# Kernel optimization log

Measured on AMD Instinct MI355X. Metric: run time of the kernel, lower is better.

Reference implementation:

```python
import jax, jax.numpy as jnp
import numpy as np

# dims
B, NB, T, NC = 16, 55, 512, 8          # batch, filter bands, time steps, CSP comps
D, L, H, E, K, F, C = 512, 6, 8, 8, 2, 2048, 2  # embed, depth, heads, experts, top_k, d_ff, classes
DH = D // H
IN = NB * NC  # 440
EPS = 1e-5


def _ln(x, s, b):
    m = x.mean(-1, keepdims=True)
    v = ((x - m) ** 2).mean(-1, keepdims=True)
    return (x - m) / jnp.sqrt(v + EPS) * s + b


def setup_inputs() -> dict:
    key = jax.random.key(0)
    ks = iter(jax.random.split(key, 64))
    n = lambda shape, s=0.02: jax.random.normal(next(ks), shape, jnp.float32) * s
    inp = {
        "x": jax.random.normal(next(ks), (B, NB, T, NC), jnp.float32),
        # frontend
        "proj_w": n((IN, D)), "proj_b": jnp.zeros((D,), jnp.float32),
        "pos": n((1, T, D)),
        "ln_pre_s": jnp.ones((D,), jnp.float32), "ln_pre_b": jnp.zeros((D,), jnp.float32),
        # stacked transformer-block params [L, ...]
        "ln1_s": jnp.ones((L, D), jnp.float32), "ln1_b": jnp.zeros((L, D), jnp.float32),
        "wq": n((L, D, D)), "bq": jnp.zeros((L, D), jnp.float32),
        "wk": n((L, D, D)), "bk": jnp.zeros((L, D), jnp.float32),
        "wv": n((L, D, D)), "bv": jnp.zeros((L, D), jnp.float32),
        "wo": n((L, D, D)), "bo": jnp.zeros((L, D), jnp.float32),
        "ln2_s": jnp.ones((L, D), jnp.float32), "ln2_b": jnp.zeros((L, D), jnp.float32),
        "gate_w": n((L, D, E)),
        "e_w1": n((L, E, D, F)), "e_b1": jnp.zeros((L, E, F), jnp.float32),
        "e_w2": n((L, E, F, D)), "e_b2": jnp.zeros((L, E, D), jnp.float32),
        # classifier head
        "ln_f_s": jnp.ones((D,), jnp.float32), "ln_f_b": jnp.zeros((D,), jnp.float32),
        "head_w": n((D, C)), "head_b": jnp.zeros((C,), jnp.float32),
    }
    return inp


def _moe(h, gw, w1, b1, w2, b2):
    # h: [N, D]; top-K softmax-gated mixture of GELU-FFN experts + load-balance aux loss
    N = h.shape[0]
    probs = jax.nn.softmax(h @ gw, axis=-1)                  # [N, E]
    vals, idx = jax.lax.top_k(probs, K)                      # [N, K]
    w = vals / vals.sum(-1, keepdims=True)                   # renormalized top-k weights
    disp = jax.nn.one_hot(idx, E, dtype=h.dtype)             # [N, K, E]
    combine = (disp * w[..., None]).sum(1)                   # [N, E]
    y = jnp.zeros_like(h)
    for e in range(E):  # small fixed expert loop
        y = y + combine[:, e:e + 1] * (jax.nn.gelu(h @ w1[e] + b1[e]) @ w2[e] + b2[e])
    frac = disp.mean((0, 1)) * K                             # fraction of tokens routed to each expert
    aux = E * jnp.sum(frac * probs.mean(0))
    return y, aux


def reference(x, proj_w, proj_b, pos, ln_pre_s, ln_pre_b, ln1_s, ln1_b, wq, bq, wk, bk,
              wv, bv, wo, bo, ln2_s, ln2_b, gate_w, e_w1, e_b1, e_w2, e_b2,
              ln_f_s, ln_f_b, head_w, head_b):
    b, nb, t, nc = x.shape
    h = x.transpose(0, 2, 1, 3).reshape(b, t, nb * nc) @ proj_w + proj_b  # [B,T,D]
    h = _ln(h + pos[:, :t, :], ln_pre_s, ln_pre_b)
    scale = DH ** -0.5
    total_aux = jnp.float32(0.0)
    for l in range(L):
        # pre-LN multi-head self-attention
        a = _ln(h, ln1_s[l], ln1_b[l])
        q = (a @ wq[l] + bq[l]).reshape(b, t, H, DH)
        k = (a @ wk[l] + bk[l]).reshape(b, t, H, DH)
        v = (a @ wv[l] + bv[l]).reshape(b, t, H, DH)
        att = jax.nn.softmax(jnp.einsum('bqhd,bkhd->bhqk', q, k) * scale, axis=-1)
        o = jnp.einsum('bhqk,bkhd->bqhd', att, v).reshape(b, t, D) @ wo[l] + bo[l]
        h = h + o
        # pre-LN MoE FFN
        m = _ln(h, ln2_s[l], ln2_b[l]).reshape(b * t, D)
        y, aux = _moe(m, gate_w[l], e_w1[l], e_b1[l], e_w2[l], e_b2[l])
        h = h + y.reshape(b, t, D)
        total_aux = total_aux + aux
    pooled = h.mean(axis=1)                                   # [B, D]
    logits = _ln(pooled, ln_f_s, ln_f_b) @ head_w + head_b    # [B, C]
    return logits, total_aux
```

## Files before the change

### kernel.cpp

```cpp
#include <hip/hip_runtime.h>
#include <stdint.h>

typedef unsigned short u16;
typedef unsigned int   u32;
typedef short bh8 __attribute__((ext_vector_type(8)));
typedef float f4  __attribute__((ext_vector_type(4)));

#define NTOK    8192
#define PADROWS 17408
#define MAXTILES 136

__device__ __forceinline__ u16 f2bf(float f){
  u32 u = __float_as_uint(f);
  return (u16)((u + 0x7fffu + ((u>>16)&1u)) >> 16);
}
__device__ __forceinline__ float bf2f(u16 h){ return __uint_as_float(((u32)h)<<16); }
__device__ __forceinline__ u32 pk2(float a, float b){ return (u32)f2bf(a) | ((u32)f2bf(b)<<16); }
__device__ __forceinline__ float gelu_f(float x){
  float u = 0.7978845608028654f*(x + 0.044715f*x*x*x);
  float t = 1.f - 2.f/(__expf(2.f*u)+1.f);
  return 0.5f*x*(1.f+t);
}
__device__ __forceinline__ void gload_lds16(const void* g, void* l){
  __builtin_amdgcn_global_load_lds((const __attribute__((address_space(1))) u32*)g,
                                   (__attribute__((address_space(3))) u32*)l, 16, 0, 0);
}

__global__ __launch_bounds__(256) void xpose_k(const float* __restrict__ x, u16* __restrict__ xt){
  int idx = blockIdx.x*256 + threadIdx.x;
  const float* src = x + (size_t)idx*8;
  float4 a = *(const float4*)src;
  float4 b = *(const float4*)(src+4);
  int t  = idx & 511;
  int nb = (idx>>9) % 55;
  int bb = (idx>>9) / 55;
  uint4 u;
  u.x = pk2(a.x,a.y); u.y = pk2(a.z,a.w); u.z = pk2(b.x,b.y); u.w = pk2(b.z,b.w);
  *(uint4*)&xt[((size_t)(bb*512+t))*448 + nb*8] = u;
}

__device__ __forceinline__ void tile_xpose(const float* __restrict__ src, u16* __restrict__ dst,
                                           int Ksrc, int N, int Kdst, float (*tile)[65])
{
  int tid = threadIdx.x;
  int k0 = blockIdx.y*64, n0 = blockIdx.x*64;
  #pragma unroll
  for (int p=0;p<4;++p){
    int r = p*16 + (tid>>4);
    int c4 = (tid&15)*4;
    int k = k0 + r;
    float4 v = (k < Ksrc) ? *(const float4*)&src[(size_t)k*N + n0 + c4] : (float4){0.f,0.f,0.f,0.f};
    tile[r][c4]=v.x; tile[r][c4+1]=v.y; tile[r][c4+2]=v.z; tile[r][c4+3]=v.w;
  }
  __syncthreads();
  #pragma unroll
  for (int p=0;p<2;++p){
    int rn = p*32 + (tid>>3);
    int ck = (tid&7)*8;
    uint4 u;
    u.x = pk2(tile[ck+0][rn], tile[ck+1][rn]);
    u.y = pk2(tile[ck+2][rn], tile[ck+3][rn]);
    u.z = pk2(tile[ck+4][rn], tile[ck+5][rn]);
    u.w = pk2(tile[ck+6][rn], tile[ck+7][rn]);
    *(uint4*)&dst[(size_t)(n0+rn)*Kdst + k0 + ck] = u;
  }
}

__global__ __launch_bounds__(256) void wconv_k(const float* __restrict__ src, u16* __restrict__ dst,
                                               int Ksrc, int N, int Kdst){
  __shared__ float tile[64][65];
  src += (size_t)blockIdx.z*Ksrc*N;
  dst += (size_t)blockIdx.z*N*Kdst;
  tile_xpose(src, dst, Ksrc, N, Kdst, tile);
}

__global__ __launch_bounds__(256) void wconv4_k(const float* __restrict__ wq, const float* __restrict__ wk,
    const float* __restrict__ wv, const float* __restrict__ wo,
    u16* __restrict__ qkvt, u16* __restrict__ wot)
{
  __shared__ float tile[64][65];
  int z = blockIdx.z;
  const float* src = (z==0)? wq : (z==1)? wk : (z==2)? wv : wo;
  u16* dst = (z==3) ? wot : qkvt + (size_t)z*512*512;
  tile_xpose(src, dst, 512, 512, 512, tile);
}

__global__ __launch_bounds__(256) void qkvb_k(const float* __restrict__ bq, const float* __restrict__ bk,
                                              const float* __restrict__ bv, float* __restrict__ qkvb){
  int idx = blockIdx.x*256 + threadIdx.x;
  int l = idx/1536, c = idx - l*1536;
  const float* s = (c<512)? bq : (c<1024)? bk : bv;
  qkvb[idx] = s[l*512 + (c&511)];
}

template<int MODE, bool GATHER>
__global__ __launch_bounds__(256) void gemm2_k(
    const u16* __restrict__ A, int lda,
    const u16* __restrict__ Bt, int ldb, int Ksteps,
    const float* __restrict__ biasBase,
    float* __restrict__ Cf, u16* __restrict__ Cb, int ldc,
    const int* __restrict__ tile_e, const int* __restrict__ toklist,
    const int* __restrict__ slotk, const float* __restrict__ wlist,
    int expN)
{
  __shared__ __align__(16) u16 As[128*32];
  __shared__ __align__(16) u16 Bs[128*32];
  const int tid = threadIdx.x, lane = tid&63, w = tid>>6;
  const int wr = w>>1, wc = w&1;
  const int n0 = blockIdx.x*128, m0 = blockIdx.y*128;
  const u16* Bp = Bt;
  const float* bias = biasBase;
  if constexpr (MODE>=3){
    int e = tile_e[blockIdx.y];
    Bp   += (size_t)e*(size_t)expN*(size_t)ldb;
    bias += (size_t)e*(size_t)expN;
  }
  const u16* asrc0; const u16* asrc1; const u16* bsrc0; const u16* bsrc1;
  {
    int idx0 = tid, row0 = idx0>>2, sp0 = idx0&3, ks0 = sp0 ^ ((row0>>1)&3);
    int idx1 = 256+tid, row1 = idx1>>2, sp1 = idx1&3, ks1 = sp1 ^ ((row1>>1)&3);
    size_t ar0 = GATHER ? (size_t)toklist[m0+row0] : (size_t)(m0+row0);
    size_t ar1 = GATHER ? (size_t)toklist[m0+row1] : (size_t)(m0+row1);
    asrc0 = A + ar0*(size_t)lda + ks0*8;
    asrc1 = A + ar1*(size_t)lda + ks1*8;
    bsrc0 = Bp + (size_t)(n0+row0)*ldb + ks0*8;
    bsrc1 = Bp + (size_t)(n0+row1)*ldb + ks1*8;
  }
  f4 acc[4][4];
  #pragma unroll
  for (int i=0;i<4;++i)
    #pragma unroll
    for (int j=0;j<4;++j) acc[i][j] = (f4){0.f,0.f,0.f,0.f};

  for (int kt=0; kt<Ksteps; ++kt){
    gload_lds16(asrc0, &As[tid*8]);
    gload_lds16(asrc1, &As[(256+tid)*8]);
    gload_lds16(bsrc0, &Bs[tid*8]);
    gload_lds16(bsrc1, &Bs[(256+tid)*8]);
    asrc0 += 32; asrc1 += 32; bsrc0 += 32; bsrc1 += 32;
    __syncthreads();
    bh8 af[4], bf[4];
    const int q = lane>>4;
    #pragma unroll
    for (int mf=0;mf<4;++mf){
      int r = wr*64 + mf*16 + (lane&15);
      af[mf] = *(const bh8*)&As[r*32 + (q ^ ((r>>1)&3))*8];
    }
    #pragma unroll
    for (int nf=0;nf<4;++nf){
      int r = wc*64 + nf*16 + (lane&15);
      bf[nf] = *(const bh8*)&Bs[r*32 + (q ^ ((r>>1)&3))*8];
    }
    #pragma unroll
    for (int mf=0;mf<4;++mf)
      #pragma unroll
      for (int nf=0;nf<4;++nf)
        acc[mf][nf] = __builtin_amdgcn_mfma_f32_16x16x32_bf16(af[mf], bf[nf], acc[mf][nf], 0, 0, 0);
    __syncthreads();
  }
  #pragma unroll
  for (int mf=0;mf<4;++mf){
    #pragma unroll
    for (int nf=0;nf<4;++nf){
      f4 d = acc[mf][nf];
      int ncol = n0 + wc*64 + nf*16 + (lane&15);
      float bv = bias[ncol];
      #pragma unroll
      for (int r=0;r<4;++r){
        int mrow = m0 + wr*64 + mf*16 + (lane>>4)*4 + r;
        float val = d[r] + bv;
        if constexpr (MODE==0){
          Cf[(size_t)mrow*ldc + ncol] = val;
        } else if constexpr (MODE==1){
          int slab = ncol>>6, dh = ncol&63;
          Cb[((size_t)slab*NTOK + (size_t)mrow)*64 + dh] = f2bf(val);
        } else if constexpr (MODE==2){
          Cf[(size_t)mrow*ldc + ncol] += val;
        } else if constexpr (MODE==3){
          Cb[(size_t)mrow*ldc + ncol] = f2bf(gelu_f(val));
        } else {
          int sk = slotk[mrow];
          if (sk >= 0){
            int tok = toklist[mrow];
            atomicAdd(&Cf[(size_t)tok*512 + ncol], wlist[mrow]*val);
          }
        }
      }
    }
  }
}

template<bool ADDPOS, bool OUTF32>
__global__ __launch_bounds__(256) void ln_k(const float* __restrict__ X, const float* __restrict__ pos,
    const float* __restrict__ sc, const float* __restrict__ bi,
    float* __restrict__ outF, u16* __restrict__ outB)
{
  int tid=threadIdx.x, lane=tid&63, w=tid>>6;
  int row = blockIdx.x*4 + w;
  const float* xr = X + (size_t)row*512 + lane*8;
  float x[8];
  float4 v0 = *(const float4*)xr;
  float4 v1 = *(const float4*)(xr+4);
  x[0]=v0.x;x[1]=v0.y;x[2]=v0.z;x[3]=v0.w;x[4]=v1.x;x[5]=v1.y;x[6]=v1.z;x[7]=v1.w;
  if constexpr (ADDPOS){
    const float* pr = pos + (size_t)(row&511)*512 + lane*8;
    float4 p0 = *(const float4*)pr, p1 = *(const float4*)(pr+4);
    x[0]+=p0.x;x[1]+=p0.y;x[2]+=p0.z;x[3]+=p0.w;x[4]+=p1.x;x[5]+=p1.y;x[6]+=p1.z;x[7]+=p1.w;
  }
  float sm=0.f, sq=0.f;
  #pragma unroll
  for (int i=0;i<8;++i){ sm+=x[i]; sq+=x[i]*x[i]; }
  #pragma unroll
  for (int mk=1; mk<64; mk<<=1){ sm += __shfl_xor(sm, mk); sq += __shfl_xor(sq, mk); }
  float mean = sm*(1.f/512.f);
  float var  = sq*(1.f/512.f) - mean*mean;
  float rstd = rsqrtf(var + 1e-5f);
  int d0 = lane*8;
  float4 s0 = *(const float4*)(sc+d0), s1 = *(const float4*)(sc+d0+4);
  float4 b0 = *(const float4*)(bi+d0), b1 = *(const float4*)(bi+d0+4);
  float y[8];
  y[0]=(x[0]-mean)*rstd*s0.x+b0.x; y[1]=(x[1]-mean)*rstd*s0.y+b0.y;
  y[2]=(x[2]-mean)*rstd*s0.z+b0.z; y[3]=(x[3]-mean)*rstd*s0.w+b0.w;
  y[4]=(x[4]-mean)*rstd*s1.x+b1.x; y[5]=(x[5]-mean)*rstd*s1.y+b1.y;
  y[6]=(x[6]-mean)*rstd*s1.z+b1.z; y[7]=(x[7]-mean)*rstd*s1.w+b1.w;
  if constexpr (OUTF32){
    float4 o0 = {y[0],y[1],y[2],y[3]}, o1 = {y[4],y[5],y[6],y[7]};
    *(float4*)(outF + (size_t)row*512 + d0)     = o0;
    *(float4*)(outF + (size_t)row*512 + d0 + 4) = o1;
  } else {
    uint4 u; u.x=pk2(y[0],y[1]); u.y=pk2(y[2],y[3]); u.z=pk2(y[4],y[5]); u.w=pk2(y[6],y[7]);
    *(uint4*)&outB[(size_t)row*512 + d0] = u;
  }
}

__global__ __launch_bounds__(256) void attn_k(const u16* __restrict__ QKV, u16* __restrict__ Og)
{
  __shared__ __align__(16) u16 VT[2][64*72];
  __shared__ __align__(16) u16 PS[4][16*72];
  int tid=threadIdx.x, lane=tid&63, w=tid>>6;
  int qt=blockIdx.x, hh=blockIdx.y, bb=blockIdx.z;
  const u16* Qh = QKV + ((size_t)hh     *NTOK + (size_t)bb*512)*64;
  const u16* Kh = QKV + ((size_t)(8+hh) *NTOK + (size_t)bb*512)*64;
  const u16* Vh = QKV + ((size_t)(16+hh)*NTOK + (size_t)bb*512)*64;
  size_t obase = (size_t)bb*512*512 + (size_t)hh*64;
  int qrow0 = qt*64 + w*16;
  bh8 qf[2];
  #pragma unroll
  for (int kf=0;kf<2;++kf)
    qf[kf] = *(const bh8*)&Qh[ (size_t)(qrow0 + (lane&15))*64 + kf*32 + (lane>>4)*8 ];
  f4 oacc[4];
  #pragma unroll
  for (int i=0;i<4;++i) oacc[i] = (f4){0.f,0.f,0.f,0.f};
  float mrun[4] = {-1e30f,-1e30f,-1e30f,-1e30f};
  float lrun[4] = {0.f,0.f,0.f,0.f};
  const float scale = 0.125f;

  for (int kt=0; kt<8; ++kt){
    const int buf = kt&1;
    #pragma unroll
    for (int r2=0;r2<2;++r2){
      int idx = r2*256 + tid;
      int dhg = idx&7;
      int dh0 = dhg*8, key = idx>>3;
      uint4 raw = *(const uint4*)&Vh[ (size_t)(kt*64+key)*64 + dh0 ];
      int kx = key ^ (dhg<<3);
      u32 rw[4] = {raw.x, raw.y, raw.z, raw.w};
      #pragma unroll
      for (int j=0;j<4;++j){
        VT[buf][(dh0+2*j  )*72 + kx] = (u16)(rw[j]&0xffff);
        VT[buf][(dh0+2*j+1)*72 + kx] = (u16)(rw[j]>>16);
      }
    }
    f4 s[4];
    #pragma unroll
    for (int nf=0;nf<4;++nf){
      size_t krow = (size_t)(kt*64+nf*16+(lane&15))*64 + (lane>>4)*8;
      bh8 k0 = *(const bh8*)&Kh[krow];
      bh8 k1 = *(const bh8*)&Kh[krow+32];
      f4 z = (f4){0.f,0.f,0.f,0.f};
      z = __builtin_amdgcn_mfma_f32_16x16x32_bf16(qf[0], k0, z, 0,0,0);
      z = __builtin_amdgcn_mfma_f32_16x16x32_bf16(qf[1], k1, z, 0,0,0);
      s[nf] = z;
    }
    float pe[4][4];
    #pragma unroll
    for (int r=0;r<4;++r){
      float sv0=s[0][r]*scale, sv1=s[1][r]*scale, sv2=s[2][r]*scale, sv3=s[3][r]*scale;
      float mt = fmaxf(fmaxf(sv0,sv1), fmaxf(sv2,sv3));
      #pragma unroll
      for (int mk=1; mk<16; mk<<=1) mt = fmaxf(mt, __shfl_xor(mt, mk));
      float mn = fmaxf(mrun[r], mt);
      float sf = __expf(mrun[r]-mn);
      float p0=__expf(sv0-mn), p1=__expf(sv1-mn), p2=__expf(sv2-mn), p3=__expf(sv3-mn);
      pe[0][r]=p0; pe[1][r]=p1; pe[2][r]=p2; pe[3][r]=p3;
      float rs = p0+p1+p2+p3;
      #pragma unroll
      for (int mk=1; mk<16; mk<<=1) rs += __shfl_xor(rs, mk);
      lrun[r] = lrun[r]*sf + rs;
      mrun[r] = mn;
      #pragma unroll
      for (int df=0;df<4;++df) oacc[df][r] *= sf;
    }
    #pragma unroll
    for (int nf=0;nf<4;++nf)
      #pragma unroll
      for (int r=0;r<4;++r)
        PS[w][ ((lane>>4)*4+r)*72 + nf*16 + (lane&15) ] = f2bf(pe[nf][r]);
    __syncthreads();
    #pragma unroll
    for (int ks=0;ks<2;++ks){
      bh8 pa = *(const bh8*)&PS[w][ (lane&15)*72 + ks*32 + (lane>>4)*8 ];
      #pragma unroll
      for (int df=0;df<4;++df){
        int dh = df*16 + (lane&15);
        int sgrp = (dh>>3)&7;
        bh8 vb = *(const bh8*)&VT[buf][ dh*72 + ((ks*4 + (lane>>4)) ^ sgrp)*8 ];
        oacc[df] = __builtin_amdgcn_mfma_f32_16x16x32_bf16(pa, vb, oacc[df], 0,0,0);
      }
    }
  }
  #pragma unroll
  for (int df=0;df<4;++df)
    #pragma unroll
    for (int r=0;r<4;++r){
      int qr = qrow0 + (lane>>4)*4 + r;
      float ov = oacc[df][r] / lrun[r];
      Og[ obase + (size_t)qr*512 + df*16 + (lane&15) ] = f2bf(ov);
    }
}

__global__ __launch_bounds__(256) void route_k(const u16* __restrict__ m, const float* __restrict__ gw,
    float* __restrict__ psum, int* __restrict__ cnt, int* __restrict__ t2e, float* __restrict__ t2w)
{
  __shared__ float ps[8]; __shared__ int cs[8];
  int tid=threadIdx.x, lane=tid&63, w=tid>>6;
  if (tid<8){ ps[tid]=0.f; cs[tid]=0; }
  __syncthreads();
  for (int it=0; it<4; ++it){
    int t = blockIdx.x*16 + w*4 + it;
    const u16* row = m + (size_t)t*512 + lane*8;
    uint4 raw = *(const uint4*)row;
    u32 rw[4] = {raw.x,raw.y,raw.z,raw.w};
    float x[8];
    #pragma unroll
    for (int j=0;j<4;++j){ x[2*j]=bf2f((u16)(rw[j]&0xffff)); x[2*j+1]=bf2f((u16)(rw[j]>>16)); }
    float acc[8] = {0,0,0,0,0,0,0,0};
    #pragma unroll
    for (int j=0;j<8;++j){
      const float* g = gw + (size_t)(lane*8+j)*8;
      float4 g0 = *(const float4*)g, g1 = *(const float4*)(g+4);
      acc[0]+=x[j]*g0.x; acc[1]+=x[j]*g0.y; acc[2]+=x[j]*g0.z; acc[3]+=x[j]*g0.w;
      acc[4]+=x[j]*g1.x; acc[5]+=x[j]*g1.y; acc[6]+=x[j]*g1.z; acc[7]+=x[j]*g1.w;
    }
    #pragma unroll
    for (int mk=1; mk<64; mk<<=1)
      #pragma unroll
      for (int e=0;e<8;++e) acc[e] += __shfl_xor(acc[e], mk);
    if (lane==0){
      float mx=acc[0];
      #pragma unroll
      for (int e=1;e<8;++e) mx = fmaxf(mx, acc[e]);
      float pe[8], tot=0.f;
      #pragma unroll
      for (int e=0;e<8;++e){ pe[e]=__expf(acc[e]-mx); tot+=pe[e]; }
      float inv = 1.f/tot;
      #pragma unroll
      for (int e=0;e<8;++e) pe[e]*=inv;
      int e0=0; float v0=pe[0];
      #pragma unroll
      for (int e=1;e<8;++e) if (pe[e]>v0){ v0=pe[e]; e0=e; }
      int e1=-1; float v1=-1.f;
      #pragma unroll
      for (int e=0;e<8;++e) if (e!=e0 && pe[e]>v1){ v1=pe[e]; e1=e; }
      float invw = 1.f/(v0+v1);
      t2e[2*t]=e0; t2w[2*t]=v0*invw; t2e[2*t+1]=e1; t2w[2*t+1]=v1*invw;
      #pragma unroll
      for (int e=0;e<8;++e) atomicAdd(&ps[e], pe[e]);
      atomicAdd(&cs[e0],1); atomicAdd(&cs[e1],1);
    }
  }
  __syncthreads();
  if (tid<8){ atomicAdd(&psum[tid], ps[tid]); atomicAdd(&cnt[tid], cs[tid]); }
}

__global__ __launch_bounds__(256) void offsets_k(const int* __restrict__ cnt, const float* __restrict__ psum,
    int* __restrict__ offs, int* __restrict__ fill, int* __restrict__ tile_e,
    int* __restrict__ toklist, int* __restrict__ slotk, float* __restrict__ wlist, float* __restrict__ auxp)
{
  int tid = threadIdx.x;
  if (tid==0){
    int off=0; float auxl=0.f;
    for (int e=0;e<8;++e){
      offs[e] = off;
      int reg = (cnt[e]+127)&~127;
      int t0 = off>>7, t1 = (off+reg)>>7;
      for (int t=t0;t<t1;++t) tile_e[t]=e;
      off += reg;
      auxl += ((float)cnt[e]*(1.f/8192.f)) * (psum[e]*(1.f/8192.f));
    }
    for (int t=off>>7; t<MAXTILES; ++t) tile_e[t]=0;
    auxp[0] += 8.f*auxl;
  }
  if (tid<8) fill[tid]=0;
  for (int i=tid;i<PADROWS;i+=256){ toklist[i]=0; slotk[i]=-1; wlist[i]=0.f; }
}

__global__ __launch_bounds__(256) void scatter_k(const int* __restrict__ t2e, const float* __restrict__ t2w,
    const int* __restrict__ offs, int* __restrict__ fill,
    int* __restrict__ toklist, int* __restrict__ slotk, float* __restrict__ wlist)
{
  int t = blockIdx.x*256 + threadIdx.x;
  #pragma unroll
  for (int kk=0;kk<2;++kk){
    int e = t2e[2*t+kk];
    int p = atomicAdd(&fill[e], 1);
    int i = offs[e] + p;
    toklist[i] = t; slotk[i] = kk; wlist[i] = t2w[2*t+kk];
  }
}

__global__ __launch_bounds__(256) void pool_k(const float* __restrict__ h, float* __restrict__ pooled){
  int idx = blockIdx.x*256 + threadIdx.x;
  int bb = idx>>9, d = idx&511;
  const float* p = h + (size_t)bb*512*512 + d;
  float s=0.f;
  for (int t=0;t<512;++t) s += p[(size_t)t*512];
  pooled[idx] = s*(1.f/512.f);
}

__global__ __launch_bounds__(256) void head_k(const float* __restrict__ pooled,
    const float* __restrict__ sc, const float* __restrict__ bi,
    const float* __restrict__ hw, const float* __restrict__ hb,
    const float* __restrict__ auxp, float* __restrict__ out)
{
  int tid=threadIdx.x, lane=tid&63, w=tid>>6;
  for (int i=0;i<4;++i){
    int row = w*4+i;
    const float* xr = pooled + (size_t)row*512 + lane*8;
    float x[8];
    float4 v0 = *(const float4*)xr, v1 = *(const float4*)(xr+4);
    x[0]=v0.x;x[1]=v0.y;x[2]=v0.z;x[3]=v0.w;x[4]=v1.x;x[5]=v1.y;x[6]=v1.z;x[7]=v1.w;
    float sm=0.f, sq=0.f;
    #pragma unroll
    for (int j=0;j<8;++j){ sm+=x[j]; sq+=x[j]*x[j]; }
    #pragma unroll
    for (int mk=1; mk<64; mk<<=1){ sm += __shfl_xor(sm, mk); sq += __shfl_xor(sq, mk); }
    float mean = sm*(1.f/512.f);
    float rstd = rsqrtf(sq*(1.f/512.f) - mean*mean + 1e-5f);
    int d0 = lane*8;
    float c0=0.f, c1=0.f;
    #pragma unroll
    for (int j=0;j<8;++j){
      float yv = (x[j]-mean)*rstd*sc[d0+j] + bi[d0+j];
      c0 += yv*hw[(d0+j)*2]; c1 += yv*hw[(d0+j)*2+1];
    }
    #pragma unroll
    for (int mk=1; mk<64; mk<<=1){ c0 += __shfl_xor(c0, mk); c1 += __shfl_xor(c1, mk); }
    if (lane==0){ out[row*2+0] = c0 + hb[0]; out[row*2+1] = c1 + hb[1]; }
  }
  if (tid==0) out[32] = auxp[0];
}

extern "C" void kernel_launch(void* const* d_in, const int* in_sizes, int n_in,
                              void* d_out, int out_size, void* d_ws, size_t ws_size,
                              hipStream_t stream)
{
  (void)in_sizes; (void)n_in; (void)out_size; (void)ws_size;
  const float* x      = (const float*)d_in[0];
  const float* proj_w = (const float*)d_in[1];
  const float* proj_b = (const float*)d_in[2];
  const float* pos    = (const float*)d_in[3];
  const float* ln_pre_s=(const float*)d_in[4];
  const float* ln_pre_b=(const float*)d_in[5];
  const float* ln1_s  = (const float*)d_in[6];
  const float* ln1_b  = (const float*)d_in[7];
  const float* wq     = (const float*)d_in[8];
  const float* bq     = (const float*)d_in[9];
  const float* wk     = (const float*)d_in[10];
  const float* bk     = (const float*)d_in[11];
  const float* wv     = (const float*)d_in[12];
  const float* bv     = (const float*)d_in[13];
  const float* wo     = (const float*)d_in[14];
  const float* bo     = (const float*)d_in[15];
  const float* ln2_s  = (const float*)d_in[16];
  const float* ln2_b  = (const float*)d_in[17];
  const float* gate_w = (const float*)d_in[18];
  const float* e_w1   = (const float*)d_in[19];
  const float* e_b1   = (const float*)d_in[20];
  const float* e_w2   = (const float*)d_in[21];
  const float* e_b2   = (const float*)d_in[22];
  const float* ln_f_s = (const float*)d_in[23];
  const float* ln_f_b = (const float*)d_in[24];
  const float* head_w = (const float*)d_in[25];
  const float* head_b = (const float*)d_in[26];

  char* base = (char*)d_ws;
  size_t off = 0;
  auto carve = [&](size_t bytes)->char*{
    char* r = base + off; off += (bytes + 255) & ~(size_t)255; return r;
  };
  u16*   xt      = (u16*)  carve((size_t)8192*448*2);
  float* h       = (float*)carve((size_t)8192*512*4);
  u16*   a       = (u16*)  carve((size_t)8192*512*2);
  u16*   qkv     = (u16*)  carve((size_t)8192*1536*2);
  u16*   ob      = (u16*)  carve((size_t)8192*512*2);
  u16*   hidden  = (u16*)  carve((size_t)PADROWS*2048*2);
  u16*   projt   = (u16*)  carve((size_t)512*448*2);
  u16*   qkvt    = (u16*)  carve((size_t)1536*512*2);
  u16*   wot     = (u16*)  carve((size_t)512*512*2);
  u16*   w1t     = (u16*)  carve((size_t)8*2048*512*2);
  u16*   w2t     = (u16*)  carve((size_t)8*512*2048*2);
  float* qkvb    = (float*)carve((size_t)6*1536*4);
  int*   toklist = (int*)  carve(PADROWS*4);
  int*   slotk   = (int*)  carve(PADROWS*4);
  float* wlist   = (float*)carve(PADROWS*4);
  int*   tile_e  = (int*)  carve(256*4);
  int*   rcnt    = (int*)  carve(96);
  float* psum    = (float*)(rcnt+8);
  int*   fill    = rcnt+16;
  int*   offs    = (int*)  carve(64);
  int*   t2e     = (int*)  carve(16384*4);
  float* t2w     = (float*)carve(16384*4);
  float* pooled  = (float*)carve(8192*4);
  float* auxp    = (float*)carve(256);

  hipMemsetAsync(xt, 0, (size_t)8192*448*2, stream);
  hipMemsetAsync(auxp, 0, 4, stream);

  xpose_k<<<1760, 256, 0, stream>>>(x, xt);
  wconv_k<<<dim3(8,7,1), 256, 0, stream>>>(proj_w, projt, 440, 512, 448);
  qkvb_k<<<36, 256, 0, stream>>>(bq, bk, bv, qkvb);
  gemm2_k<0,false><<<dim3(4,64), 256, 0, stream>>>(xt, 448, projt, 448, 14, proj_b,
      h, nullptr, 512, nullptr, nullptr, nullptr, nullptr, 0);
  ln_k<true,true><<<2048, 256, 0, stream>>>(h, pos, ln_pre_s, ln_pre_b, h, nullptr);

  for (int l=0; l<6; ++l){
    wconv4_k<<<dim3(8,8,4), 256, 0, stream>>>(wq+(size_t)l*512*512, wk+(size_t)l*512*512,
        wv+(size_t)l*512*512, wo+(size_t)l*512*512, qkvt, wot);
    ln_k<false,false><<<2048, 256, 0, stream>>>(h, nullptr, ln1_s+(size_t)l*512, ln1_b+(size_t)l*512, nullptr, a);
    gemm2_k<1,false><<<dim3(12,64), 256, 0, stream>>>(a, 512, qkvt, 512, 16, qkvb+(size_t)l*1536,
        nullptr, qkv, 1536, nullptr, nullptr, nullptr, nullptr, 0);
    attn_k<<<dim3(8,8,16), 256, 0, stream>>>(qkv, ob);
    gemm2_k<2,false><<<dim3(4,64), 256, 0, stream>>>(ob, 512, wot, 512, 16, bo+(size_t)l*512,
        h, nullptr, 512, nullptr, nullptr, nullptr, nullptr, 0);
    ln_k<false,false><<<2048, 256, 0, stream>>>(h, nullptr, ln2_s+(size_t)l*512, ln2_b+(size_t)l*512, nullptr, a);
    hipMemsetAsync(rcnt, 0, 64, stream);
    route_k<<<512, 256, 0, stream>>>(a, gate_w+(size_t)l*512*8, psum, rcnt, t2e, t2w);
    offsets_k<<<1, 256, 0, stream>>>(rcnt, psum, offs, fill, tile_e, toklist, slotk, wlist, auxp);
    scatter_k<<<32, 256, 0, stream>>>(t2e, t2w, offs, fill, toklist, slotk, wlist);
    wconv_k<<<dim3(32,8,8), 256, 0, stream>>>(e_w1+(size_t)l*8*512*2048, w1t, 512, 2048, 512);
    wconv_k<<<dim3(8,32,8), 256, 0, stream>>>(e_w2+(size_t)l*8*2048*512, w2t, 2048, 512, 2048);
    gemm2_k<3,true ><<<dim3(16,MAXTILES), 256, 0, stream>>>(a, 512, w1t, 512, 16,
        e_b1 + (size_t)l*8*2048, nullptr, hidden, 2048, tile_e, toklist, slotk, wlist, 2048);
    gemm2_k<4,false><<<dim3(4,MAXTILES), 256, 0, stream>>>(hidden, 2048, w2t, 2048, 64,
        e_b2 + (size_t)l*8*512, h, nullptr, 512, tile_e, toklist, slotk, wlist, 512);
  }

  pool_k<<<32, 256, 0, stream>>>(h, pooled);
  head_k<<<1, 256, 0, stream>>>(pooled, ln_f_s, ln_f_b, head_w, head_b, auxp, (float*)d_out);
}
```

Before: 2.475 ms.

## Replace MoE atomic scatter-add with bf16 expert output buffer and gather kernel

New measurement: 2.417 ms. 1.02x faster.

```diff
diff --git a/kernel.cpp b/kernel.cpp
--- a/kernel.cpp
+++ b/kernel.cpp
@@ -100,18 +100,23 @@
     const float* __restrict__ biasBase,
     float* __restrict__ Cf, u16* __restrict__ Cb, int ldc,
     const int* __restrict__ tile_e, const int* __restrict__ toklist,
-    const int* __restrict__ slotk, const float* __restrict__ wlist,
-    int expN)
+    const float* __restrict__ wlist, int expN)
 {
   __shared__ __align__(16) u16 As[128*32];
   __shared__ __align__(16) u16 Bs[128*32];
   const int tid = threadIdx.x, lane = tid&63, w = tid>>6;
   const int wr = w>>1, wc = w&1;
-  const int n0 = blockIdx.x*128, m0 = blockIdx.y*128;
+  int nx = gridDim.x;
+  int nwg = nx * gridDim.y;
+  int lin = blockIdx.y*nx + blockIdx.x;
+  int qq = nwg>>3, rr = nwg&7, xc = lin&7, oo = lin>>3;
+  int wg = (xc<rr ? xc*(qq+1) : rr*(qq+1)+(xc-rr)*qq) + oo;
+  int by = wg/nx, bx = wg - by*nx;
+  const int n0 = bx*128, m0 = by*128;
   const u16* Bp = Bt;
   const float* bias = biasBase;
   if constexpr (MODE>=3){
-    int e = tile_e[blockIdx.y];
+    int e = tile_e[by];
     Bp   += (size_t)e*(size_t)expN*(size_t)ldb;
     bias += (size_t)e*(size_t)expN;
   }
@@ -179,11 +184,7 @@
         } else if constexpr (MODE==3){
           Cb[(size_t)mrow*ldc + ncol] = f2bf(gelu_f(val));
         } else {
-          int sk = slotk[mrow];
-          if (sk >= 0){
-            int tok = toklist[mrow];
-            atomicAdd(&Cf[(size_t)tok*512 + ncol], wlist[mrow]*val);
-          }
+          Cb[(size_t)mrow*ldc + ncol] = f2bf(wlist[mrow]*val);
         }
       }
     }
@@ -385,7 +386,7 @@
 
 __global__ __launch_bounds__(256) void offsets_k(const int* __restrict__ cnt, const float* __restrict__ psum,
     int* __restrict__ offs, int* __restrict__ fill, int* __restrict__ tile_e,
-    int* __restrict__ toklist, int* __restrict__ slotk, float* __restrict__ wlist, float* __restrict__ auxp)
+    int* __restrict__ toklist, float* __restrict__ wlist, float* __restrict__ auxp)
 {
   int tid = threadIdx.x;
   if (tid==0){
@@ -402,12 +403,12 @@
     auxp[0] += 8.f*auxl;
   }
   if (tid<8) fill[tid]=0;
-  for (int i=tid;i<PADROWS;i+=256){ toklist[i]=0; slotk[i]=-1; wlist[i]=0.f; }
+  for (int i=tid;i<PADROWS;i+=256){ toklist[i]=0; wlist[i]=0.f; }
 }
 
 __global__ __launch_bounds__(256) void scatter_k(const int* __restrict__ t2e, const float* __restrict__ t2w,
     const int* __restrict__ offs, int* __restrict__ fill,
-    int* __restrict__ toklist, int* __restrict__ slotk, float* __restrict__ wlist)
+    int* __restrict__ toklist, float* __restrict__ wlist, int* __restrict__ t2pos)
 {
   int t = blockIdx.x*256 + threadIdx.x;
   #pragma unroll
@@ -415,8 +416,30 @@
     int e = t2e[2*t+kk];
     int p = atomicAdd(&fill[e], 1);
     int i = offs[e] + p;
-    toklist[i] = t; slotk[i] = kk; wlist[i] = t2w[2*t+kk];
-  }
+    toklist[i] = t; wlist[i] = t2w[2*t+kk]; t2pos[2*t+kk] = i;
+  }
+}
+
+__global__ __launch_bounds__(256) void gather_k(float* __restrict__ h, const u16* __restrict__ yb,
+                                                const int* __restrict__ t2pos)
+{
+  int tid = threadIdx.x;
+  int t = blockIdx.x*4 + (tid>>6);
+  int lane = tid&63;
+  int p0 = t2pos[2*t], p1 = t2pos[2*t+1];
+  uint4 a = *(const uint4*)&yb[(size_t)p0*512 + lane*8];
+  uint4 b = *(const uint4*)&yb[(size_t)p1*512 + lane*8];
+  float* hp = h + (size_t)t*512 + lane*8;
+  float4 h0 = *(float4*)hp, h1 = *(float4*)(hp+4);
+  h0.x += bf2f((u16)(a.x&0xffff)) + bf2f((u16)(b.x&0xffff));
+  h0.y += bf2f((u16)(a.x>>16))    + bf2f((u16)(b.x>>16));
+  h0.z += bf2f((u16)(a.y&0xffff)) + bf2f((u16)(b.y&0xffff));
+  h0.w += bf2f((u16)(a.y>>16))    + bf2f((u16)(b.y>>16));
+  h1.x += bf2f((u16)(a.z&0xffff)) + bf2f((u16)(b.z&0xffff));
+  h1.y += bf2f((u16)(a.z>>16))    + bf2f((u16)(b.z>>16));
+  h1.z += bf2f((u16)(a.w&0xffff)) + bf2f((u16)(b.w&0xffff));
+  h1.w += bf2f((u16)(a.w>>16))    + bf2f((u16)(b.w>>16));
+  *(float4*)hp = h0; *(float4*)(hp+4) = h1;
 }
 
 __global__ __launch_bounds__(256) void pool_k(const float* __restrict__ h, float* __restrict__ pooled){
@@ -505,6 +528,7 @@
   u16*   qkv     = (u16*)  carve((size_t)8192*1536*2);
   u16*   ob      = (u16*)  carve((size_t)8192*512*2);
   u16*   hidden  = (u16*)  carve((size_t)PADROWS*2048*2);
+  u16*   ybuf    = (u16*)  carve((size_t)PADROWS*512*2);
   u16*   projt   = (u16*)  carve((size_t)512*448*2);
   u16*   qkvt    = (u16*)  carve((size_t)1536*512*2);
   u16*   wot     = (u16*)  carve((size_t)512*512*2);
@@ -512,48 +536,50 @@
   u16*   w2t     = (u16*)  carve((size_t)8*512*2048*2);
   float* qkvb    = (float*)carve((size_t)6*1536*4);
   int*   toklist = (int*)  carve(PADROWS*4);
-  int*   slotk   = (int*)  carve(PADROWS*4);
   float* wlist   = (float*)carve(PADROWS*4);
   int*   tile_e  = (int*)  carve(256*4);
-  int*   rcnt    = (int*)  carve(96);
-  float* psum    = (float*)(rcnt+8);
-  int*   fill    = rcnt+16;
+  int*   rcntA   = (int*)  carve(6*16*4);
+  int*   fill    = (int*)  carve(64);
   int*   offs    = (int*)  carve(64);
   int*   t2e     = (int*)  carve(16384*4);
   float* t2w     = (float*)carve(16384*4);
+  int*   t2pos   = (int*)  carve(16384*4);
   float* pooled  = (float*)carve(8192*4);
   float* auxp    = (float*)carve(256);
 
   hipMemsetAsync(xt, 0, (size_t)8192*448*2, stream);
+  hipMemsetAsync(rcntA, 0, 6*16*4, stream);
   hipMemsetAsync(auxp, 0, 4, stream);
 
   xpose_k<<<1760, 256, 0, stream>>>(x, xt);
   wconv_k<<<dim3(8,7,1), 256, 0, stream>>>(proj_w, projt, 440, 512, 448);
   qkvb_k<<<36, 256, 0, stream>>>(bq, bk, bv, qkvb);
   gemm2_k<0,false><<<dim3(4,64), 256, 0, stream>>>(xt, 448, projt, 448, 14, proj_b,
-      h, nullptr, 512, nullptr, nullptr, nullptr, nullptr, 0);
+      h, nullptr, 512, nullptr, nullptr, nullptr, 0);
   ln_k<true,true><<<2048, 256, 0, stream>>>(h, pos, ln_pre_s, ln_pre_b, h, nullptr);
 
   for (int l=0; l<6; ++l){
+    int*   cnt  = rcntA + l*16;
+    float* psum = (float*)(cnt + 8);
     wconv4_k<<<dim3(8,8,4), 256, 0, stream>>>(wq+(size_t)l*512*512, wk+(size_t)l*512*512,
         wv+(size_t)l*512*512, wo+(size_t)l*512*512, qkvt, wot);
     ln_k<false,false><<<2048, 256, 0, stream>>>(h, nullptr, ln1_s+(size_t)l*512, ln1_b+(size_t)l*512, nullptr, a);
     gemm2_k<1,false><<<dim3(12,64), 256, 0, stream>>>(a, 512, qkvt, 512, 16, qkvb+(size_t)l*1536,
-        nullptr, qkv, 1536, nullptr, nullptr, nullptr, nullptr, 0);
+        nullptr, qkv, 1536, nullptr, nullptr, nullptr, 0);
     attn_k<<<dim3(8,8,16), 256, 0, stream>>>(qkv, ob);
     gemm2_k<2,false><<<dim3(4,64), 256, 0, stream>>>(ob, 512, wot, 512, 16, bo+(size_t)l*512,
-        h, nullptr, 512, nullptr, nullptr, nullptr, nullptr, 0);
+        h, nullptr, 512, nullptr, nullptr, nullptr, 0);
     ln_k<false,false><<<2048, 256, 0, stream>>>(h, nullptr, ln2_s+(size_t)l*512, ln2_b+(size_t)l*512, nullptr, a);
-    hipMemsetAsync(rcnt, 0, 64, stream);
-    route_k<<<512, 256, 0, stream>>>(a, gate_w+(size_t)l*512*8, psum, rcnt, t2e, t2w);
-    offsets_k<<<1, 256, 0, stream>>>(rcnt, psum, offs, fill, tile_e, toklist, slotk, wlist, auxp);
-    scatter_k<<<32, 256, 0, stream>>>(t2e, t2w, offs, fill, toklist, slotk, wlist);
+    route_k<<<512, 256, 0, stream>>>(a, gate_w+(size_t)l*512*8, psum, cnt, t2e, t2w);
+    offsets_k<<<1, 256, 0, stream>>>(cnt, psum, offs, fill, tile_e, toklist, wlist, auxp);
+    scatter_k<<<32, 256, 0, stream>>>(t2e, t2w, offs, fill, toklist, wlist, t2pos);
     wconv_k<<<dim3(32,8,8), 256, 0, stream>>>(e_w1+(size_t)l*8*512*2048, w1t, 512, 2048, 512);
     wconv_k<<<dim3(8,32,8), 256, 0, stream>>>(e_w2+(size_t)l*8*2048*512, w2t, 2048, 512, 2048);
     gemm2_k<3,true ><<<dim3(16,MAXTILES), 256, 0, stream>>>(a, 512, w1t, 512, 16,
-        e_b1 + (size_t)l*8*2048, nullptr, hidden, 2048, tile_e, toklist, slotk, wlist, 2048);
+        e_b1 + (size_t)l*8*2048, nullptr, hidden, 2048, tile_e, toklist, wlist, 2048);
     gemm2_k<4,false><<<dim3(4,MAXTILES), 256, 0, stream>>>(hidden, 2048, w2t, 2048, 64,
-        e_b2 + (size_t)l*8*512, h, nullptr, 512, tile_e, toklist, slotk, wlist, 512);
+        e_b2 + (size_t)l*8*512, nullptr, ybuf, 512, tile_e, nullptr, wlist, 512);
+    gather_k<<<2048, 256, 0, stream>>>(h, ybuf, t2pos);
   }
 
   pool_k<<<32, 256, 0, stream>>>(h, pooled);
```
